# Kernel tuning notes

Hardware: AMD Instinct MI355X
Metric: run time of the kernel (lower is better)

The kernel has to match this reference:

```python
import jax, jax.numpy as jnp
import numpy as np


def _lstm(x, Wx, Wh, b):
    """Fused-gate LSTM over time axis 1. x: [B,T,I]; Wx: [I,4H]; Wh: [H,4H]; b: [4H].
    Gate order (i, f, g, o) as in flax.linen.LSTMCell. Zero initial carry."""
    B, T, _ = x.shape
    H = Wh.shape[0]
    # Precompute all input-to-gate contributions in one big GEMM.
    xg = jnp.einsum('bti,ih->bth', x, Wx) + b  # [B,T,4H]

    def step(carry, xt):
        c, h = carry
        z = xt + h @ Wh  # [B,4H]
        i, f, g, o = jnp.split(z, 4, axis=-1)
        c = jax.nn.sigmoid(f) * c + jax.nn.sigmoid(i) * jnp.tanh(g)
        h = jax.nn.sigmoid(o) * jnp.tanh(c)
        return (c, h), h

    init = (jnp.zeros((B, H), x.dtype), jnp.zeros((B, H), x.dtype))
    _, hs = jax.lax.scan(step, init, jnp.swapaxes(xg, 0, 1))  # hs: [T,B,H]
    return jnp.swapaxes(hs, 0, 1)  # [B,T,H]


def _forward(X, conv_w, conv_b,
             Wx1, Wh1, b1, Wx2, Wh2, b2, Wx3, Wh3, b3, Wx4, Wh4, b4,
             Wa, ba, Va, bva, Wd1, bd1, Wd2, bd2):
    # 1-D conv, SAME padding (flax default), NWC layout.
    x = jax.lax.conv_general_dilated(X, conv_w, (1,), 'SAME',
                                     dimension_numbers=('NWC', 'WIO', 'NWC')) + conv_b
    # NOTE: source uses jnp.flip(..., axis=-1) -> flips FEATURE axis (faithful to source).
    x1 = _lstm(x, Wx1, Wh1, b1)
    x2 = _lstm(jnp.flip(x, axis=-1), Wx2, Wh2, b2)
    x = jnp.concatenate([x1, x2], axis=-1)  # [B,T,2F]
    x1 = _lstm(x, Wx3, Wh3, b3)
    x2 = _lstm(jnp.flip(x, axis=-1), Wx4, Wh4, b4)
    enc = jnp.concatenate([x1, x2], axis=-1)  # [B,T,4F]
    # Additive attention: softmax over time axis.
    score = jnp.tanh(enc @ Wa + ba) @ Va + bva  # [B,T,1]
    w = jax.nn.softmax(score, axis=1)
    ctx = jnp.sum(w * enc, axis=1)  # [B,4F]
    # MLP head (dropout deterministic -> identity).
    h = jnp.tanh(ctx @ Wd1 + bd1)
    return h @ Wd2 + bd2  # [B,1]


def setup_inputs() -> dict:
    key = jax.random.key(0)
    B, T, Cin, F = 32, 4096, 8, 64
    ks = iter(jax.random.split(key, 32))

    def w(shape):
        fan_in = shape[0] if len(shape) <= 2 else shape[0] * shape[1]
        return jax.random.normal(next(ks), shape, jnp.float32) / np.sqrt(fan_in)

    d = {}
    d['X'] = jax.random.normal(next(ks), (B, T, Cin), jnp.float32)
    d['conv_w'] = w((4, Cin, 16))
    d['conv_b'] = jnp.zeros((16,), jnp.float32)
    lstm_dims = {'1': (16, F), '2': (16, F), '3': (2 * F, 2 * F), '4': (2 * F, 2 * F)}
    for n, (i_dim, h_dim) in lstm_dims.items():
        d['Wx' + n] = w((i_dim, 4 * h_dim))
        d['Wh' + n] = w((h_dim, 4 * h_dim))
        d['b' + n] = jnp.zeros((4 * h_dim,), jnp.float32)
    d['Wa'] = w((4 * F, F)); d['ba'] = jnp.zeros((F,), jnp.float32)
    d['Va'] = w((F, 1));     d['bva'] = jnp.zeros((1,), jnp.float32)
    d['Wd1'] = w((4 * F, F)); d['bd1'] = jnp.zeros((F,), jnp.float32)
    d['Wd2'] = w((F, 1));     d['bd2'] = jnp.zeros((1,), jnp.float32)
    d['deterministic'] = 1
    return d


def reference(X, conv_w, conv_b,
              Wx1, Wh1, b1, Wx2, Wh2, b2, Wx3, Wh3, b3, Wx4, Wh4, b4,
              Wa, ba, Va, bva, Wd1, bd1, Wd2, bd2, deterministic):
    # deterministic=1 -> dropout is the identity; already reflected in _forward.
    return _forward(X, conv_w, conv_b,
                    Wx1, Wh1, b1, Wx2, Wh2, b2, Wx3, Wh3, b3, Wx4, Wh4, b4,
                    Wa, ba, Va, bva, Wd1, bd1, Wd2, bd2)
```

## Files before the change

kernel.cpp:

```cpp
#include <hip/hip_runtime.h>


#define TFULL 4096
#define NB 32

__device__ __forceinline__ float fexp2(float x){ return __builtin_amdgcn_exp2f(x); }
__device__ __forceinline__ float frcp(float x){ return __builtin_amdgcn_rcpf(x); }
__device__ __forceinline__ float sigf(float x){ return frcp(1.f + fexp2(-1.44269504f*x)); }
__device__ __forceinline__ float tanh_(float x){
    float e = fexp2(fminf(2.88539008f*x, 126.f));
    return (e - 1.f) * frcp(e + 1.f);
}
#define PIN4(v) asm volatile("" : "+v"(v.x), "+v"(v.y), "+v"(v.z), "+v"(v.w))

__global__ __launch_bounds__(256) void k_init(float* __restrict__ st1,
        float* __restrict__ st2, float* __restrict__ am, float* __restrict__ al,
        float* __restrict__ acc){
    int i = blockIdx.x * 256 + threadIdx.x;
    if (i < 8192)  st1[i] = 0.f;
    if (i < 16384) st2[i] = 0.f;
    if (i < 8192)  acc[i] = 0.f;
    if (i < 32){ am[i] = -3.4e38f; al[i] = 0.f; }
}

__global__ __launch_bounds__(256) void k_pack(
        const float* __restrict__ Wx1, const float* __restrict__ Wh1, const float* __restrict__ b1,
        const float* __restrict__ Wx2, const float* __restrict__ Wh2, const float* __restrict__ b2,
        const float* __restrict__ Wx3, const float* __restrict__ Wh3, const float* __restrict__ b3,
        const float* __restrict__ Wx4, const float* __restrict__ Wh4, const float* __restrict__ b4,
        float* __restrict__ W34, float* __restrict__ b34, float* __restrict__ W2p,
        float* __restrict__ W1p, float* __restrict__ b12i){
    int i0 = blockIdx.x * 256 + threadIdx.x;
    int stride = gridDim.x * 256;
    for (int e = i0; e < 131072; e += stride){
        int k = e >> 10, n = e & 1023;
        int l = n >> 9, nn = n & 511, j = nn >> 2, g = nn & 3;
        W34[e] = l ? Wx4[(127 - k)*512 + g*128 + j] : Wx3[k*512 + g*128 + j];
    }
    for (int e = i0; e < 1024; e += stride){
        int l = e >> 9, nn = e & 511, j = nn >> 2, g = nn & 3;
        b34[e] = (l ? b4 : b3)[g*128 + j];
    }
    for (int e = i0; e < 131072; e += stride){
        int l = e >> 16, r = e & 65535, tid = r >> 7, widx = r & 127;
        int g = widx >> 5, kk = widx & 31;
        int wv = tid >> 6, lam = tid & 63;
        int c = lam & 15, s4 = lam >> 4;
        int J = 16*wv + c;
        W2p[e] = (l ? Wh4 : Wh3)[(32*s4 + kk)*512 + g*128 + J];
    }
    for (int e = i0; e < 40960; e += stride){
        int l = e / 20480, r = e % 20480, tid = r / 80, widx = r % 80;
        int g = widx / 20, rem = widx % 20, kk4 = rem >> 2, cmp = rem & 3;
        int wv = tid >> 6, lam = tid & 63;
        int c = lam & 15, s4 = lam >> 4;
        int J = 16*wv + c;
        float v;
        if (kk4 < 4){
            v = (l ? Wh2 : Wh1)[(16*s4 + 4*kk4 + cmp)*256 + g*64 + J];
        } else {
            int rr = 4*s4 + cmp;
            v = l ? Wx2[(15 - rr)*256 + g*64 + J] : Wx1[rr*256 + g*64 + J];
        }
        W1p[e] = v;
    }
    for (int e = i0; e < 512; e += stride){
        int l = e >> 8, nn = e & 255, j = nn >> 2, g = nn & 3;
        b12i[e] = (l ? b2 : b1)[g*64 + j];
    }
}

__global__ __launch_bounds__(256) void k_conv(const float* __restrict__ X,
        const float* __restrict__ W, const float* __restrict__ Bv,
        float* __restrict__ out, int t0, int lc){
    __shared__ float Ws[512];
    __shared__ float bs[16];
    int tid = threadIdx.x;
    Ws[tid] = W[tid]; Ws[tid + 256] = W[tid + 256];
    if (tid < 16) bs[tid] = Bv[tid];
    __syncthreads();
    int m = blockIdx.x * 256 + tid;
    int b = m >> lc, trel = m & ((1 << lc) - 1);
    int t = t0 + trel;
    float o[16];
    #pragma unroll
    for (int co = 0; co < 16; ++co) o[co] = bs[co];
    #pragma unroll
    for (int w = 0; w < 4; ++w){
        int tt = t + w - 1;
        if (tt >= 0 && tt < TFULL){
            const float* xr = X + ((size_t)(b << 12) + tt) * 8;
            #pragma unroll
            for (int ci = 0; ci < 8; ++ci){
                float v = xr[ci];
                #pragma unroll
                for (int co = 0; co < 16; ++co) o[co] += v * Ws[(w*8 + ci)*16 + co];
            }
        }
    }
    float* op = out + (size_t)m * 16;
    #pragma unroll
    for (int q = 0; q < 4; ++q)
        *(float4*)(op + q*4) = make_float4(o[q*4], o[q*4+1], o[q*4+2], o[q*4+3]);
}

__global__ void __launch_bounds__(256)
k_scan1(const float* __restrict__ x, const float* __restrict__ W1p,
        const float* __restrict__ b12i,
        float* __restrict__ cc, float* __restrict__ st1, int C){
    int l = blockIdx.x >> 5;
    int b = blockIdx.x & 31;
    int tid = threadIdx.x;
    int lam = tid & 63, wv = tid >> 6;
    int cq = lam & 15, s4 = lam >> 4;
    int J = 16*wv + cq;
    float4 w[20];
    {
        const float4* wp = (const float4*)(W1p + ((size_t)l*256 + tid)*80);
        #pragma unroll
        for (int i = 0; i < 20; ++i) w[i] = wp[i];
        #pragma unroll
        for (int i = 0; i < 20; ++i) PIN4(w[i]);
    }
    float4 bi4 = make_float4(0.f, 0.f, 0.f, 0.f);
    if (s4 == 0) bi4 = *(const float4*)(b12i + l*256 + 4*J);

    __shared__ float xs[128 * 16];
    __shared__ float ccbuf[128 * 64];
    __shared__ float hb[2][64];
    float cst = 0.f;
    int base = (l*32 + b)*64;
    if (s4 == 0) cst = st1[base + J];
    if (tid < 64) hb[0][tid] = st1[4096 + base + tid];
    __syncthreads();

    const float* xb = x + ((size_t)b * C) * 16;
    float* ccb = cc + ((size_t)b * C) * 128 + (l << 6);
    int BS = C < 128 ? C : 128;
    int bsm = BS - 1;

    #pragma clang loop unroll(disable)
    for (int t = 0; t < C; ++t){
        int st = t & bsm;
        if (st == 0){
            __syncthreads();
            if (t){
                #pragma unroll
                for (int i = 0; i < 8; ++i){
                    int Qi = tid + i*256;
                    if (Qi < BS*16){
                        int row = Qi >> 4, qr = Qi & 15;
                        *((float4*)(ccb + (size_t)(t - BS + row)*128) + qr) =
                            ((const float4*)ccbuf)[Qi];
                    }
                }
            }
            #pragma unroll
            for (int i = 0; i < 2; ++i){
                int Qi = tid + i*256;
                if (Qi < BS*4)
                    ((float4*)xs)[Qi] = ((const float4*)(xb + (size_t)t*16))[Qi];
            }
            __syncthreads();
        }
        const float* hcur = hb[t & 1];
        float a0, a1, a2, a3;
        {
            float4 xv = *(const float4*)(xs + st*16 + 4*s4);
            a0 = xv.x*w[4].x;  a0 = fmaf(xv.y, w[4].y, a0);
            a0 = fmaf(xv.z, w[4].z, a0);   a0 = fmaf(xv.w, w[4].w, a0);
            a1 = xv.x*w[9].x;  a1 = fmaf(xv.y, w[9].y, a1);
            a1 = fmaf(xv.z, w[9].z, a1);   a1 = fmaf(xv.w, w[9].w, a1);
            a2 = xv.x*w[14].x; a2 = fmaf(xv.y, w[14].y, a2);
            a2 = fmaf(xv.z, w[14].z, a2);  a2 = fmaf(xv.w, w[14].w, a2);
            a3 = xv.x*w[19].x; a3 = fmaf(xv.y, w[19].y, a3);
            a3 = fmaf(xv.z, w[19].z, a3);  a3 = fmaf(xv.w, w[19].w, a3);
        }
        #pragma unroll
        for (int k4 = 0; k4 < 4; ++k4){
            float4 hv = *(const float4*)(hcur + 16*s4 + 4*k4);
            a0 = fmaf(hv.x, w[k4].x, a0);     a0 = fmaf(hv.y, w[k4].y, a0);
            a0 = fmaf(hv.z, w[k4].z, a0);     a0 = fmaf(hv.w, w[k4].w, a0);
            a1 = fmaf(hv.x, w[5+k4].x, a1);   a1 = fmaf(hv.y, w[5+k4].y, a1);
            a1 = fmaf(hv.z, w[5+k4].z, a1);   a1 = fmaf(hv.w, w[5+k4].w, a1);
            a2 = fmaf(hv.x, w[10+k4].x, a2);  a2 = fmaf(hv.y, w[10+k4].y, a2);
            a2 = fmaf(hv.z, w[10+k4].z, a2);  a2 = fmaf(hv.w, w[10+k4].w, a2);
            a3 = fmaf(hv.x, w[15+k4].x, a3);  a3 = fmaf(hv.y, w[15+k4].y, a3);
            a3 = fmaf(hv.z, w[15+k4].z, a3);  a3 = fmaf(hv.w, w[15+k4].w, a3);
        }
        a0 += __shfl_xor(a0, 16); a0 += __shfl_xor(a0, 32);
        a1 += __shfl_xor(a1, 16); a1 += __shfl_xor(a1, 32);
        a2 += __shfl_xor(a2, 16); a2 += __shfl_xor(a2, 32);
        a3 += __shfl_xor(a3, 16); a3 += __shfl_xor(a3, 32);
        if (s4 == 0){
            float zi = a0 + bi4.x, zf = a1 + bi4.y, zg = a2 + bi4.z, zo = a3 + bi4.w;
            cst = sigf(zf) * cst + sigf(zi) * tanh_(zg);
            float h = sigf(zo) * tanh_(cst);
            hb[(t + 1) & 1][J] = h;
            ccbuf[st*64 + J] = h;
        }
        __syncthreads();
    }
    {
        #pragma unroll
        for (int i = 0; i < 8; ++i){
            int Qi = tid + i*256;
            if (Qi < BS*16){
                int row = Qi >> 4, qr = Qi & 15;
                *((float4*)(ccb + (size_t)(C - BS + row)*128) + qr) =
                    ((const float4*)ccbuf)[Qi];
            }
        }
    }
    if (s4 == 0) st1[base + J] = cst;
    if (tid < 64) st1[4096 + base + tid] = hb[C & 1][tid];
}

template<bool TANH>
__global__ __launch_bounds__(128) void k_gemm(
        const float* __restrict__ A, int lda,
        const float* __restrict__ B, int ldb,
        const float* __restrict__ bias,
        float* __restrict__ Cm, int ldc, int K){
    __shared__ float As[64 * 129];
    __shared__ float Bs[64 * 68];
    int tid = threadIdx.x;
    int tx = tid & 7;
    int ty = tid >> 3;
    int r0 = blockIdx.x * 128;
    int n0 = blockIdx.y * 64;
    float acc[8][8];
    #pragma unroll
    for (int i = 0; i < 8; ++i)
        #pragma unroll
        for (int n = 0; n < 8; ++n) acc[i][n] = 0.f;

    for (int kb = 0; kb < K; kb += 64){
        __syncthreads();
        for (int idx = tid; idx < 2048; idx += 128){
            int r = idx >> 4, k4 = idx & 15;
            float4 v = *(const float4*)(A + (size_t)(r0 + r) * lda + kb + k4*4);
            As[(k4*4 + 0)*129 + r] = v.x;
            As[(k4*4 + 1)*129 + r] = v.y;
            As[(k4*4 + 2)*129 + r] = v.z;
            As[(k4*4 + 3)*129 + r] = v.w;
        }
        for (int idx = tid; idx < 1024; idx += 128){
            int n4 = idx & 15, k = idx >> 4;
            float4 v = *(const float4*)(B + (size_t)(kb + k) * ldb + n0 + n4*4);
            *(float4*)(Bs + k*68 + n4*4) = v;
        }
        __syncthreads();
        #pragma unroll 4
        for (int k = 0; k < 64; ++k){
            float a[8];
            #pragma unroll
            for (int i = 0; i < 8; ++i) a[i] = As[k*129 + ty*8 + i];
            float4 b0 = *(const float4*)(Bs + k*68 + tx*8);
            float4 b1 = *(const float4*)(Bs + k*68 + tx*8 + 4);
            float bq[8] = {b0.x, b0.y, b0.z, b0.w, b1.x, b1.y, b1.z, b1.w};
            #pragma unroll
            for (int i = 0; i < 8; ++i)
                #pragma unroll
                for (int n = 0; n < 8; ++n) acc[i][n] += a[i] * bq[n];
        }
    }
    #pragma unroll
    for (int i = 0; i < 8; ++i){
        size_t rr = (size_t)r0 + ty*8 + i;
        float* cp = Cm + rr * ldc + n0 + tx*8;
        float ov[8];
        #pragma unroll
        for (int n = 0; n < 8; ++n){
            float v = acc[i][n] + bias[n0 + tx*8 + n];
            ov[n] = TANH ? tanh_(v) : v;
        }
        *(float4*)cp       = make_float4(ov[0], ov[1], ov[2], ov[3]);
        *(float4*)(cp + 4) = make_float4(ov[4], ov[5], ov[6], ov[7]);
    }
}

__global__ void __launch_bounds__(512)
k_scan2(const float* __restrict__ xg, const float* __restrict__ W2p,
        float* __restrict__ enc, float* __restrict__ st2, int C){
    int l = blockIdx.x >> 5;
    int b = blockIdx.x & 31;
    int tid = threadIdx.x;
    int lam = tid & 63, wv = tid >> 6;
    int cq = lam & 15, s4 = lam >> 4;
    int J = 16*wv + cq;
    float4 w[32];
    {
        const float4* wp = (const float4*)(W2p + ((size_t)l*512 + tid)*128);
        #pragma unroll
        for (int i = 0; i < 32; ++i) w[i] = wp[i];
        #pragma unroll
        for (int i = 0; i < 32; ++i) PIN4(w[i]);
    }

    __shared__ float xgbuf[32 * 512];
    __shared__ float encbuf[32 * 128];
    __shared__ float hb[2][160];
    float cst = 0.f;
    int base = (l*32 + b)*128;
    if (s4 == 0) cst = st2[base + J];
    if (tid < 128) hb[0][tid + 4*(tid >> 5)] = st2[8192 + base + tid];
    __syncthreads();

    const float* xgg = xg + ((size_t)b * C) * 1024 + (l << 9);
    float* encb = enc + ((size_t)b * C) * 256 + (l << 7);
    int hoff = 36*s4;
    int joff = J + 4*(J >> 5);

    #pragma clang loop unroll(disable)
    for (int t = 0; t < C; ++t){
        int st = t & 31;
        if (st == 0){
            __syncthreads();
            if (t){
                #pragma unroll
                for (int i = 0; i < 2; ++i){
                    int Qi = tid + i*512;
                    int row = Qi >> 5, qr = Qi & 31;
                    *((float4*)(encb + (size_t)(t - 32 + row)*256) + qr) =
                        ((const float4*)encbuf)[Qi];
                }
            }
            #pragma unroll
            for (int i = 0; i < 8; ++i){
                int Qi = tid + i*512;
                int row = Qi >> 7, qr = Qi & 127;
                ((float4*)xgbuf)[Qi] =
                    *((const float4*)(xgg + (size_t)(t + row)*1024) + qr);
            }
            __syncthreads();
        }
        const float* hcur = hb[t & 1];
        float a0 = 0.f, a1 = 0.f, a2 = 0.f, a3 = 0.f;
        #pragma unroll
        for (int k4 = 0; k4 < 8; ++k4){
            float4 hv = *(const float4*)(hcur + hoff + 4*k4);
            a0 = fmaf(hv.x, w[k4].x, a0);      a0 = fmaf(hv.y, w[k4].y, a0);
            a0 = fmaf(hv.z, w[k4].z, a0);      a0 = fmaf(hv.w, w[k4].w, a0);
            a1 = fmaf(hv.x, w[8+k4].x, a1);    a1 = fmaf(hv.y, w[8+k4].y, a1);
            a1 = fmaf(hv.z, w[8+k4].z, a1);    a1 = fmaf(hv.w, w[8+k4].w, a1);
            a2 = fmaf(hv.x, w[16+k4].x, a2);   a2 = fmaf(hv.y, w[16+k4].y, a2);
            a2 = fmaf(hv.z, w[16+k4].z, a2);   a2 = fmaf(hv.w, w[16+k4].w, a2);
            a3 = fmaf(hv.x, w[24+k4].x, a3);   a3 = fmaf(hv.y, w[24+k4].y, a3);
            a3 = fmaf(hv.z, w[24+k4].z, a3);   a3 = fmaf(hv.w, w[24+k4].w, a3);
        }
        a0 += __shfl_xor(a0, 16); a0 += __shfl_xor(a0, 32);
        a1 += __shfl_xor(a1, 16); a1 += __shfl_xor(a1, 32);
        a2 += __shfl_xor(a2, 16); a2 += __shfl_xor(a2, 32);
        a3 += __shfl_xor(a3, 16); a3 += __shfl_xor(a3, 32);
        if (s4 == 0){
            float4 xq = *(const float4*)(xgbuf + st*512 + 4*J);
            float zi = a0 + xq.x, zf = a1 + xq.y, zg = a2 + xq.z, zo = a3 + xq.w;
            cst = sigf(zf) * cst + sigf(zi) * tanh_(zg);
            float h = sigf(zo) * tanh_(cst);
            hb[(t + 1) & 1][joff] = h;
            encbuf[st*128 + J] = h;
        }
        __syncthreads();
    }
    {
        #pragma unroll
        for (int i = 0; i < 2; ++i){
            int Qi = tid + i*512;
            int row = Qi >> 5, qr = Qi & 31;
            *((float4*)(encb + (size_t)(C - 32 + row)*256) + qr) =
                ((const float4*)encbuf)[Qi];
        }
    }
    if (s4 == 0) st2[base + J] = cst;
    if (tid < 128) st2[8192 + base + tid] = hb[C & 1][tid + 4*(tid >> 5)];
}

__global__ __launch_bounds__(256) void k_scorev(const float* __restrict__ u,
        const float* __restrict__ Va, const float* __restrict__ bva,
        float* __restrict__ sc){
    int m = blockIdx.x * 256 + threadIdx.x;
    const float4* up = (const float4*)(u + (size_t)m * 64);
    const float4* vp = (const float4*)Va;
    float acc = 0.f;
    #pragma unroll
    for (int i = 0; i < 16; ++i){
        float4 v = up[i], w = vp[i];
        acc += v.x*w.x + v.y*w.y + v.z*w.z + v.w*w.w;
    }
    sc[m] = acc + bva[0];
}

__global__ __launch_bounds__(1024) void k_attn(const float* __restrict__ sc,
        const float* __restrict__ enc, float* __restrict__ am,
        float* __restrict__ al, float* __restrict__ acc, int C){
    int b = blockIdx.x, tid = threadIdx.x;
    __shared__ float es[1024];
    __shared__ float red[16];
    __shared__ float sh[2];
    const float* sp = sc + (size_t)b * C;
    float mloc = -3.4e38f;
    for (int t = tid; t < C; t += 1024) mloc = fmaxf(mloc, sp[t]);
    #pragma unroll
    for (int off = 32; off; off >>= 1) mloc = fmaxf(mloc, __shfl_down(mloc, off));
    if ((tid & 63) == 0) red[tid >> 6] = mloc;
    __syncthreads();
    if (tid == 0){
        float mc = -3.4e38f;
        #pragma unroll
        for (int i = 0; i < 16; ++i) mc = fmaxf(mc, red[i]);
        float mo = am[b];
        float mn = fmaxf(mo, mc);
        sh[0] = mn;
        sh[1] = fexp2(1.44269504f * (mo - mn));
        am[b] = mn;
    }
    __syncthreads();
    float mn = sh[0], alpha = sh[1];
    float eloc = 0.f;
    for (int t = tid; t < C; t += 1024){
        float e = fexp2(1.44269504f * (sp[t] - mn));
        es[t] = e; eloc += e;
    }
    #pragma unroll
    for (int off = 32; off; off >>= 1) eloc += __shfl_down(eloc, off);
    if ((tid & 63) == 0) red[tid >> 6] = eloc;
    __syncthreads();
    if (tid == 0){
        float sm = 0.f;
        #pragma unroll
        for (int i = 0; i < 16; ++i) sm += red[i];
        al[b] = al[b] * alpha + sm;
    }
    int jf = tid & 255, sl = tid >> 8;
    int tlen = C >> 2;
    const float* ep = enc + ((size_t)b * C + (size_t)sl * tlen) * 256 + jf;
    const float* eb = es + sl * tlen;
    float a = 0.f;
    for (int t = 0; t < tlen; ++t) a = fmaf(eb[t], ep[(size_t)t * 256], a);
    __syncthreads();
    es[tid] = a;
    __syncthreads();
    if (tid < 256)
        acc[b*256 + tid] = acc[b*256 + tid] * alpha
                         + ((es[tid] + es[256 + tid]) + (es[512 + tid] + es[768 + tid]));
}

__global__ __launch_bounds__(256) void k_head(const float* __restrict__ acc,
        const float* __restrict__ al,
        const float* __restrict__ Wd1, const float* __restrict__ bd1,
        const float* __restrict__ Wd2, const float* __restrict__ bd2,
        float* __restrict__ out){
    __shared__ float ctxs[32 * 256];
    __shared__ float h1s[32 * 64];
    int tid = threadIdx.x;
    for (int idx = tid; idx < 8192; idx += 256){
        int b = idx >> 8;
        ctxs[idx] = acc[idx] / al[b];
    }
    __syncthreads();
    for (int idx = tid; idx < 2048; idx += 256){
        int b = idx >> 6, n = idx & 63;
        float a = bd1[n];
        for (int i = 0; i < 256; ++i) a += ctxs[b*256 + i] * Wd1[i*64 + n];
        h1s[idx] = tanh_(a);
    }
    __syncthreads();
    if (tid < 32){
        float a = bd2[0];
        #pragma unroll
        for (int n = 0; n < 64; ++n) a += h1s[tid*64 + n] * Wd2[n];
        out[tid] = a;
    }
}

extern "C" void kernel_launch(void* const* d_in, const int* in_sizes, int n_in,
                              void* d_out, int out_size, void* d_ws, size_t ws_size,
                              hipStream_t stream){
    const float* X     = (const float*)d_in[0];
    const float* convw = (const float*)d_in[1];
    const float* convb = (const float*)d_in[2];
    const float* Wx1 = (const float*)d_in[3];
    const float* Wh1 = (const float*)d_in[4];
    const float* b1  = (const float*)d_in[5];
    const float* Wx2 = (const float*)d_in[6];
    const float* Wh2 = (const float*)d_in[7];
    const float* b2  = (const float*)d_in[8];
    const float* Wx3 = (const float*)d_in[9];
    const float* Wh3 = (const float*)d_in[10];
    const float* b3  = (const float*)d_in[11];
    const float* Wx4 = (const float*)d_in[12];
    const float* Wh4 = (const float*)d_in[13];
    const float* b4  = (const float*)d_in[14];
    const float* Wa  = (const float*)d_in[15];
    const float* ba  = (const float*)d_in[16];
    const float* Va  = (const float*)d_in[17];
    const float* bva = (const float*)d_in[18];
    const float* Wd1 = (const float*)d_in[19];
    const float* bd1 = (const float*)d_in[20];
    const float* Wd2 = (const float*)d_in[21];
    const float* bd2 = (const float*)d_in[22];
    float* out = (float*)d_out;
    (void)in_sizes; (void)n_in; (void)out_size;

    const size_t fixedFl = 131072 + 1024 + 131072 + 40960 + 512
                         + 8192 + 16384 + 32 + 32 + 8192 + 32*1024;
    size_t capFl = ws_size / 4;
    int C = 1024;
    while (C > 32){
        size_t need = fixedFl + (size_t)NB * C * (16 + 128 + 1024 + 256 + 64);
        if (need <= capFl) break;
        C >>= 1;
    }
    int lc = 31 - __builtin_clz((unsigned)C);
    int nch = TFULL / C;

    float* ws   = (float*)d_ws;
    float* W34  = ws;
    float* b34  = W34 + 131072;
    float* W2p  = b34 + 1024;
    float* W1p  = W2p + 131072;
    float* b12i = W1p + 40960;
    float* st1  = b12i + 512;
    float* st2  = st1 + 8192;
    float* am   = st2 + 16384;
    float* al   = am + 32;
    float* acc  = al + 32;
    float* scb  = acc + 8192;
    float* xcv  = scb + 32*1024;
    float* ccb  = xcv + (size_t)NB*C*16;
    float* xgb  = ccb + (size_t)NB*C*128;
    float* enb  = xgb + (size_t)NB*C*1024;
    float* ub   = enb + (size_t)NB*C*256;

    k_init<<<64, 256, 0, stream>>>(st1, st2, am, al, acc);
    k_pack<<<512, 256, 0, stream>>>(Wx1, Wh1, b1, Wx2, Wh2, b2,
                                    Wx3, Wh3, b3, Wx4, Wh4, b4,
                                    W34, b34, W2p, W1p, b12i);

    for (int ch = 0; ch < nch; ++ch){
        int t0 = ch * C;
        k_conv<<<NB*C/256, 256, 0, stream>>>(X, convw, convb, xcv, t0, lc);
        k_scan1<<<64, 256, 0, stream>>>(xcv, W1p, b12i, ccb, st1, C);
        k_gemm<false><<<dim3(NB*C/128, 16), 128, 0, stream>>>(
            ccb, 128, W34, 1024, b34, xgb, 1024, 128);
        k_scan2<<<64, 512, 0, stream>>>(xgb, W2p, enb, st2, C);
        k_gemm<true><<<dim3(NB*C/128, 1), 128, 0, stream>>>(
            enb, 256, Wa, 64, ba, ub, 64, 256);
        k_scorev<<<NB*C/256, 256, 0, stream>>>(ub, Va, bva, scb);
        k_attn<<<32, 1024, 0, stream>>>(scb, enb, am, al, acc, C);
    }
    k_head<<<1, 256, 0, stream>>>(acc, al, Wd1, bd1, Wd2, bd2, out);
}
```

Baseline: 6.024 ms.

## Split layer-2 LSTM recurrence across 1024 threads with DPP row reductions

The second-layer scan kernel now uses 1024 threads per block instead of 512. Each group of 8 lanes splits the 128-long hidden dot product into 16-element slices, which halves the per-thread weight registers and FMA chain on the serial critical path. Partial sums are combined with DPP row-shift adds instead of cross-row shuffles, and the weight packing, hidden-state padding and load/store loops are reworked to match. The cost is more waves taking part in each per-step barrier and only one lane in eight doing the gate math.

```diff
diff --git a/kernel.cpp b/kernel.cpp
--- a/kernel.cpp
+++ b/kernel.cpp
@@ -12,6 +12,13 @@
     return (e - 1.f) * frcp(e + 1.f);
 }
 #define PIN4(v) asm volatile("" : "+v"(v.x), "+v"(v.y), "+v"(v.z), "+v"(v.w))
+
+template<int CTRL>
+__device__ __forceinline__ float dppadd(float x){
+    int t = __builtin_amdgcn_update_dpp(0, __float_as_int(x), CTRL, 0xF, 0xF, true);
+    return x + __int_as_float(t);
+}
+#define DPPRED(a) { a = dppadd<0x111>(a); a = dppadd<0x112>(a); a = dppadd<0x114>(a); }
 
 __global__ __launch_bounds__(256) void k_init(float* __restrict__ st1,
         float* __restrict__ st2, float* __restrict__ am, float* __restrict__ al,
@@ -42,12 +49,12 @@
         b34[e] = (l ? b4 : b3)[g*128 + j];
     }
     for (int e = i0; e < 131072; e += stride){
-        int l = e >> 16, r = e & 65535, tid = r >> 7, widx = r & 127;
-        int g = widx >> 5, kk = widx & 31;
+        int l = e >> 16, r = e & 65535, tid = r >> 6, widx = r & 63;
         int wv = tid >> 6, lam = tid & 63;
-        int c = lam & 15, s4 = lam >> 4;
-        int J = 16*wv + c;
-        W2p[e] = (l ? Wh4 : Wh3)[(32*s4 + kk)*512 + g*128 + J];
+        int cq = lam >> 3, ks = lam & 7;
+        int J = 8*wv + cq;
+        int g = widx >> 4, k4 = (widx >> 2) & 3, cmp = widx & 3;
+        W2p[e] = (l ? Wh4 : Wh3)[(16*ks + 4*k4 + cmp)*512 + g*128 + J];
     }
     for (int e = i0; e < 40960; e += stride){
         int l = e / 20480, r = e % 20480, tid = r / 80, widx = r % 80;
@@ -280,22 +287,23 @@
     }
 }
 
-__global__ void __launch_bounds__(512)
+__global__ void __launch_bounds__(1024)
 k_scan2(const float* __restrict__ xg, const float* __restrict__ W2p,
         float* __restrict__ enc, float* __restrict__ st2, int C){
     int l = blockIdx.x >> 5;
     int b = blockIdx.x & 31;
     int tid = threadIdx.x;
     int lam = tid & 63, wv = tid >> 6;
-    int cq = lam & 15, s4 = lam >> 4;
-    int J = 16*wv + cq;
-    float4 w[32];
+    int cq = lam >> 3, ks = lam & 7;
+    int J = 8*wv + cq;
+    bool act = (ks == 7);
+    float4 w[16];
     {
-        const float4* wp = (const float4*)(W2p + ((size_t)l*512 + tid)*128);
-        #pragma unroll
-        for (int i = 0; i < 32; ++i) w[i] = wp[i];
-        #pragma unroll
-        for (int i = 0; i < 32; ++i) PIN4(w[i]);
+        const float4* wp = (const float4*)(W2p + ((size_t)l*1024 + tid)*64);
+        #pragma unroll
+        for (int i = 0; i < 16; ++i) w[i] = wp[i];
+        #pragma unroll
+        for (int i = 0; i < 16; ++i) PIN4(w[i]);
     }
 
     __shared__ float xgbuf[32 * 512];
@@ -303,14 +311,14 @@
     __shared__ float hb[2][160];
     float cst = 0.f;
     int base = (l*32 + b)*128;
-    if (s4 == 0) cst = st2[base + J];
-    if (tid < 128) hb[0][tid + 4*(tid >> 5)] = st2[8192 + base + tid];
+    if (act) cst = st2[base + J];
+    if (tid < 128) hb[0][tid + 4*(tid >> 4)] = st2[8192 + base + tid];
     __syncthreads();
 
     const float* xgg = xg + ((size_t)b * C) * 1024 + (l << 9);
     float* encb = enc + ((size_t)b * C) * 256 + (l << 7);
-    int hoff = 36*s4;
-    int joff = J + 4*(J >> 5);
+    int hoff = 20*ks;
+    int joff = J + 4*(J >> 4);
 
     #pragma clang loop unroll(disable)
     for (int t = 0; t < C; ++t){
@@ -318,17 +326,13 @@
         if (st == 0){
             __syncthreads();
             if (t){
-                #pragma unroll
-                for (int i = 0; i < 2; ++i){
-                    int Qi = tid + i*512;
-                    int row = Qi >> 5, qr = Qi & 31;
-                    *((float4*)(encb + (size_t)(t - 32 + row)*256) + qr) =
-                        ((const float4*)encbuf)[Qi];
-                }
+                int row = tid >> 5, qr = tid & 31;
+                *((float4*)(encb + (size_t)(t - 32 + row)*256) + qr) =
+                    ((const float4*)encbuf)[tid];
             }
             #pragma unroll
-            for (int i = 0; i < 8; ++i){
-                int Qi = tid + i*512;
+            for (int i = 0; i < 4; ++i){
+                int Qi = tid + i*1024;
                 int row = Qi >> 7, qr = Qi & 127;
                 ((float4*)xgbuf)[Qi] =
                     *((const float4*)(xgg + (size_t)(t + row)*1024) + qr);
@@ -338,42 +342,35 @@
         const float* hcur = hb[t & 1];
         float a0 = 0.f, a1 = 0.f, a2 = 0.f, a3 = 0.f;
         #pragma unroll
-        for (int k4 = 0; k4 < 8; ++k4){
+        for (int k4 = 0; k4 < 4; ++k4){
             float4 hv = *(const float4*)(hcur + hoff + 4*k4);
             a0 = fmaf(hv.x, w[k4].x, a0);      a0 = fmaf(hv.y, w[k4].y, a0);
             a0 = fmaf(hv.z, w[k4].z, a0);      a0 = fmaf(hv.w, w[k4].w, a0);
-            a1 = fmaf(hv.x, w[8+k4].x, a1);    a1 = fmaf(hv.y, w[8+k4].y, a1);
-            a1 = fmaf(hv.z, w[8+k4].z, a1);    a1 = fmaf(hv.w, w[8+k4].w, a1);
-            a2 = fmaf(hv.x, w[16+k4].x, a2);   a2 = fmaf(hv.y, w[16+k4].y, a2);
-            a2 = fmaf(hv.z, w[16+k4].z, a2);   a2 = fmaf(hv.w, w[16+k4].w, a2);
-            a3 = fmaf(hv.x, w[24+k4].x, a3);   a3 = fmaf(hv.y, w[24+k4].y, a3);
-            a3 = fmaf(hv.z, w[24+k4].z, a3);   a3 = fmaf(hv.w, w[24+k4].w, a3);
-        }
-        a0 += __shfl_xor(a0, 16); a0 += __shfl_xor(a0, 32);
-        a1 += __shfl_xor(a1, 16); a1 += __shfl_xor(a1, 32);
-        a2 += __shfl_xor(a2, 16); a2 += __shfl_xor(a2, 32);
-        a3 += __shfl_xor(a3, 16); a3 += __shfl_xor(a3, 32);
-        if (s4 == 0){
-            float4 xq = *(const float4*)(xgbuf + st*512 + 4*J);
+            a1 = fmaf(hv.x, w[4+k4].x, a1);    a1 = fmaf(hv.y, w[4+k4].y, a1);
+            a1 = fmaf(hv.z, w[4+k4].z, a1);    a1 = fmaf(hv.w, w[4+k4].w, a1);
+            a2 = fmaf(hv.x, w[8+k4].x, a2);    a2 = fmaf(hv.y, w[8+k4].y, a2);
+            a2 = fmaf(hv.z, w[8+k4].z, a2);    a2 = fmaf(hv.w, w[8+k4].w, a2);
+            a3 = fmaf(hv.x, w[12+k4].x, a3);   a3 = fmaf(hv.y, w[12+k4].y, a3);
+            a3 = fmaf(hv.z, w[12+k4].z, a3);   a3 = fmaf(hv.w, w[12+k4].w, a3);
+        }
+        DPPRED(a0); DPPRED(a1); DPPRED(a2); DPPRED(a3);
+        if (act){
+            float4 xq = *(const float4*)(xgbuf + (st << 9) + 4*J);
             float zi = a0 + xq.x, zf = a1 + xq.y, zg = a2 + xq.z, zo = a3 + xq.w;
             cst = sigf(zf) * cst + sigf(zi) * tanh_(zg);
             float h = sigf(zo) * tanh_(cst);
             hb[(t + 1) & 1][joff] = h;
-            encbuf[st*128 + J] = h;
+            encbuf[(st << 7) + J] = h;
         }
         __syncthreads();
     }
     {
-        #pragma unroll
-        for (int i = 0; i < 2; ++i){
-            int Qi = tid + i*512;
-            int row = Qi >> 5, qr = Qi & 31;
-            *((float4*)(encb + (size_t)(C - 32 + row)*256) + qr) =
-                ((const float4*)encbuf)[Qi];
-        }
-    }
-    if (s4 == 0) st2[base + J] = cst;
-    if (tid < 128) st2[8192 + base + tid] = hb[C & 1][tid + 4*(tid >> 5)];
+        int row = tid >> 5, qr = tid & 31;
+        *((float4*)(encb + (size_t)(C - 32 + row)*256) + qr) =
+            ((const float4*)encbuf)[tid];
+    }
+    if (act) st2[base + J] = cst;
+    if (tid < 128) st2[8192 + base + tid] = hb[C & 1][tid + 4*(tid >> 4)];
 }
 
 __global__ __launch_bounds__(256) void k_scorev(const float* __restrict__ u,
@@ -544,7 +541,7 @@
         k_scan1<<<64, 256, 0, stream>>>(xcv, W1p, b12i, ccb, st1, C);
         k_gemm<false><<<dim3(NB*C/128, 16), 128, 0, stream>>>(
             ccb, 128, W34, 1024, b34, xgb, 1024, 128);
-        k_scan2<<<64, 512, 0, stream>>>(xgb, W2p, enb, st2, C);
+        k_scan2<<<64, 1024, 0, stream>>>(xgb, W2p, enb, st2, C);
         k_gemm<true><<<dim3(NB*C/128, 1), 128, 0, stream>>>(
             enb, 256, Wa, 64, ba, ub, 64, 256);
         k_scorev<<<NB*C/256, 256, 0, stream>>>(ub, Va, bva, scb);
```

Result: slower. 6.233 ms (+3.5%).
